# Kernel tuning notes

Hardware: AMD Instinct MI355X
Metric: run time of the kernel (lower is better)

The kernel has to match this reference:

```python
import jax, jax.numpy as jnp
import numpy as np

B, S, D, E, K = 4, 4096, 2048, 64, 8

def setup_inputs() -> dict:
    key = jax.random.key(0)
    k1, k2 = jax.random.split(key, 2)
    x = jax.random.normal(k1, (B, S, D), dtype=jnp.float32)
    # centroid projection params (Dense(features=n_experts))
    W = jax.random.normal(k2, (D, E), dtype=jnp.float32) / np.sqrt(D).astype(np.float32)
    b = jnp.zeros((E,), dtype=jnp.float32)
    return {"x": x, "W": W, "b": b, "k": K}

def reference(x, W, b, k):
    # dense gating projection + sigmoid -> per-token expert scores [B,S,E]
    scores = jax.nn.sigmoid(jnp.einsum('bsd,de->bse', x, W) + b)
    # per-token top-k expert selection (vectorized form of apply_along_axis(top))
    g_i, idx = jax.lax.top_k(scores, k)          # [B,S,k]
    g = g_i / jnp.sum(g_i, axis=-1, keepdims=True)  # renormalize top-k gates
    return g, idx, scores
```

## Files before the change

kernel.cpp:

```cpp
#include <hip/hip_runtime.h>
#include <math.h>
#include <stdint.h>

#define NTOK   16384
#define DDIM   2048
#define NE     64
#define TOPK   8

#define THREADS 512
#define NWAVE   8
#define TOKPB   32
#define BK      64
#define NCHUNK  (DDIM / BK)
#define KSLICE  (BK / NWAVE)

#define XSLOTS   ((BK / 4) * TOKPB)
#define WSLOTS   (BK * (NE / 4))
#define BUFSLOTS (XSLOTS + WSLOTS)

#define SBIDX(t,e) ((t)*67 + ((e) ^ ((t) & 7)))

__device__ __forceinline__ void gl_lds16(const void* g, void* l) {
    __builtin_amdgcn_global_load_lds(
        (const __attribute__((address_space(1))) void*)(uintptr_t)g,
        (__attribute__((address_space(3))) void*)(uintptr_t)l,
        16, 0, 0);
}

__global__ __launch_bounds__(THREADS, 2) void gate_kernel(
    const float* __restrict__ x, const float* __restrict__ W,
    const float* __restrict__ b, float* __restrict__ out)
{
    __shared__ float4 smem[2 * BUFSLOTS];

    const int tid  = threadIdx.x;
    const int wave = tid >> 6;
    const int lane = tid & 63;
    const int tg   = lane >> 3;
    const int eg   = lane & 7;
    const int tok0 = blockIdx.x * TOKPB;

    const int st_k4 = tid >> 5;
    const int st_sg = lane & 31;
    const int st_t  = 4 * (st_sg & 7) + (st_sg >> 3);
    const float* gx  = x + (size_t)(tok0 + st_t) * DDIM + st_k4 * 4;
    const float* gw0 = W + (size_t)(wave * 128 + lane) * 4;
    const float* gw1 = gw0 + 64 * 4;

    float acc[4][8];
#pragma unroll
    for (int i = 0; i < 4; ++i)
#pragma unroll
        for (int j = 0; j < 8; ++j) acc[i][j] = 0.f;

    auto stage = [&](int c) {
        float4* B = &smem[(c & 1) * BUFSLOTS];
        const int kc = c * BK;
        gl_lds16(gx + kc,             &B[wave * 64]);
        gl_lds16(gw0 + (size_t)kc * NE, &B[XSLOTS + wave * 128]);
        gl_lds16(gw1 + (size_t)kc * NE, &B[XSLOTS + wave * 128 + 64]);
    };

    stage(0);
    __syncthreads();

    for (int c = 0; c < NCHUNK; ++c) {
        if (c + 1 < NCHUNK) stage(c + 1);
        const float4* BX = &smem[(c & 1) * BUFSLOTS];
        const float4* BW = BX + XSLOTS;
#pragma unroll
        for (int g = 0; g < 2; ++g) {
            const int k4 = wave * 2 + g;
            float4 xv[4];
#pragma unroll
            for (int i = 0; i < 4; ++i)
                xv[i] = BX[k4 * 32 + tg + 8 * i];
#pragma unroll
            for (int kk = 0; kk < 4; ++kk) {
                const int k = k4 * 4 + kk;
                const float4 wa = BW[k * 16 + eg * 2];
                const float4 wb = BW[k * 16 + eg * 2 + 1];
                const float ws[8] = {wa.x, wa.y, wa.z, wa.w,
                                     wb.x, wb.y, wb.z, wb.w};
#pragma unroll
                for (int i = 0; i < 4; ++i) {
                    const float xs = ((const float*)&xv[i])[kk];
#pragma unroll
                    for (int j = 0; j < 8; ++j)
                        acc[i][j] = fmaf(xs, ws[j], acc[i][j]);
                }
            }
        }
        __syncthreads();
    }

    float* sb = (float*)smem;
    for (int s = tid; s < TOKPB * 67; s += THREADS) sb[s] = 0.f;
    __syncthreads();
#pragma unroll
    for (int i = 0; i < 4; ++i)
#pragma unroll
        for (int j = 0; j < 8; ++j)
            atomicAdd(&sb[SBIDX(tg * 4 + i, eg * 8 + j)], acc[i][j]);
    __syncthreads();

    float* out_g   = out;
    float* out_idx = out + (size_t)NTOK * TOPK;
    float* out_s   = out + (size_t)NTOK * TOPK * 2;

#pragma unroll
    for (int r = 0; r < (TOKPB * NE) / THREADS; ++r) {
        const int flat = r * THREADS + tid;
        const int t = flat >> 6;
        const int e = flat & 63;
        const float z = sb[SBIDX(t, e)] + b[e];
        const float s = 1.f / (1.f + expf(-z));
        out_s[(size_t)tok0 * NE + flat] = s;
        sb[SBIDX(t, e)] = s;
    }
    __syncthreads();

    if (tid < TOKPB) {
        const int t = tid;
        float gv[TOPK];
        int   gi[TOPK];
        float sum = 0.f;
#pragma unroll
        for (int j = 0; j < TOPK; ++j) {
            float best = -1.f;
            int bi = 0;
            for (int e = 0; e < NE; ++e) {
                const float v = sb[SBIDX(t, e)];
                if (v > best) { best = v; bi = e; }
            }
            gv[j] = best; gi[j] = bi; sum += best;
            sb[SBIDX(t, bi)] = -2.f;
        }
        const float inv = 1.f / sum;
#pragma unroll
        for (int j = 0; j < TOPK; ++j) {
            out_g[(size_t)(tok0 + t) * TOPK + j]   = gv[j] * inv;
            out_idx[(size_t)(tok0 + t) * TOPK + j] = (float)gi[j];
        }
    }
}

extern "C" void kernel_launch(void* const* d_in, const int* in_sizes, int n_in,
                              void* d_out, int out_size, void* d_ws, size_t ws_size,
                              hipStream_t stream) {
    const float* x = (const float*)d_in[0];
    const float* W = (const float*)d_in[1];
    const float* b = (const float*)d_in[2];
    float* out = (float*)d_out;
    gate_kernel<<<NTOK / TOKPB, THREADS, 0, stream>>>(x, W, b, out);
}
```

Before: 262.2 us.

## Split k-slices across half-waves with 8x8 per-thread register tile and swizzled W

```diff
diff --git a/kernel.cpp b/kernel.cpp
--- a/kernel.cpp
+++ b/kernel.cpp
@@ -12,10 +12,9 @@
 #define TOKPB   32
 #define BK      64
 #define NCHUNK  (DDIM / BK)
-#define KSLICE  (BK / NWAVE)
 
-#define XSLOTS   ((BK / 4) * TOKPB)
-#define WSLOTS   (BK * (NE / 4))
+#define XSLOTS   512
+#define WSLOTS   1024
 #define BUFSLOTS (XSLOTS + WSLOTS)
 
 #define SBIDX(t,e) ((t)*67 + ((e) ^ ((t) & 7)))
@@ -36,29 +35,33 @@
     const int tid  = threadIdx.x;
     const int wave = tid >> 6;
     const int lane = tid & 63;
-    const int tg   = lane >> 3;
+    const int half = lane >> 5;
+    const int tg   = (lane >> 3) & 3;
     const int eg   = lane & 7;
+    const int k4   = wave * 2 + half;
     const int tok0 = blockIdx.x * TOKPB;
 
-    const int st_k4 = tid >> 5;
-    const int st_sg = lane & 31;
-    const int st_t  = 4 * (st_sg & 7) + (st_sg >> 3);
-    const float* gx  = x + (size_t)(tok0 + st_t) * DDIM + st_k4 * 4;
-    const float* gw0 = W + (size_t)(wave * 128 + lane) * 4;
-    const float* gw1 = gw0 + 64 * 4;
+    const int st_t = (tid & 3) * 8 + ((tid >> 2) & 7);
+    const float* gx = x + (size_t)(tok0 + st_t) * DDIM + ((tid >> 5) << 2);
+    const int s0 = wave * 128 + lane;
+    const int k0 = s0 >> 4, e40 = (s0 & 15) ^ ((k0 >> 2) & 1);
+    const int s1 = s0 + 64;
+    const int k1 = s1 >> 4, e41 = (s1 & 15) ^ ((k1 >> 2) & 1);
+    const float* gw0 = W + (size_t)k0 * NE + e40 * 4;
+    const float* gw1 = W + (size_t)k1 * NE + e41 * 4;
 
-    float acc[4][8];
+    float acc[8][8];
 #pragma unroll
-    for (int i = 0; i < 4; ++i)
+    for (int i = 0; i < 8; ++i)
 #pragma unroll
         for (int j = 0; j < 8; ++j) acc[i][j] = 0.f;
 
     auto stage = [&](int c) {
         float4* B = &smem[(c & 1) * BUFSLOTS];
         const int kc = c * BK;
-        gl_lds16(gx + kc,             &B[wave * 64]);
-        gl_lds16(gw0 + (size_t)kc * NE, &B[XSLOTS + wave * 128]);
-        gl_lds16(gw1 + (size_t)kc * NE, &B[XSLOTS + wave * 128 + 64]);
+        gl_lds16(gx + kc,                    &B[wave * 64]);
+        gl_lds16(gw0 + (size_t)kc * NE,      &B[XSLOTS + wave * 128]);
+        gl_lds16(gw1 + (size_t)kc * NE,      &B[XSLOTS + wave * 128 + 64]);
     };
 
     stage(0);
@@ -68,27 +71,25 @@
         if (c + 1 < NCHUNK) stage(c + 1);
         const float4* BX = &smem[(c & 1) * BUFSLOTS];
         const float4* BW = BX + XSLOTS;
+
+        float4 xv[8];
 #pragma unroll
-        for (int g = 0; g < 2; ++g) {
-            const int k4 = wave * 2 + g;
-            float4 xv[4];
+        for (int i = 0; i < 8; ++i)
+            xv[i] = BX[k4 * 32 + i * 4 + tg];
+
 #pragma unroll
-            for (int i = 0; i < 4; ++i)
-                xv[i] = BX[k4 * 32 + tg + 8 * i];
+        for (int kk = 0; kk < 4; ++kk) {
+            const int k = k4 * 4 + kk;
+            const float4 wa = BW[k * 16 + eg * 2 + half];
+            const float4 wb = BW[k * 16 + eg * 2 + 1 - half];
+            const float ws[8] = {wa.x, wa.y, wa.z, wa.w,
+                                 wb.x, wb.y, wb.z, wb.w};
 #pragma unroll
-            for (int kk = 0; kk < 4; ++kk) {
-                const int k = k4 * 4 + kk;
-                const float4 wa = BW[k * 16 + eg * 2];
-                const float4 wb = BW[k * 16 + eg * 2 + 1];
-                const float ws[8] = {wa.x, wa.y, wa.z, wa.w,
-                                     wb.x, wb.y, wb.z, wb.w};
+            for (int i = 0; i < 8; ++i) {
+                const float xs = ((const float*)&xv[i])[kk];
 #pragma unroll
-                for (int i = 0; i < 4; ++i) {
-                    const float xs = ((const float*)&xv[i])[kk];
-#pragma unroll
-                    for (int j = 0; j < 8; ++j)
-                        acc[i][j] = fmaf(xs, ws[j], acc[i][j]);
-                }
+                for (int j = 0; j < 8; ++j)
+                    acc[i][j] = fmaf(xs, ws[j], acc[i][j]);
             }
         }
         __syncthreads();
@@ -98,10 +99,10 @@
     for (int s = tid; s < TOKPB * 67; s += THREADS) sb[s] = 0.f;
     __syncthreads();
 #pragma unroll
-    for (int i = 0; i < 4; ++i)
+    for (int i = 0; i < 8; ++i)
 #pragma unroll
         for (int j = 0; j < 8; ++j)
-            atomicAdd(&sb[SBIDX(tg * 4 + i, eg * 8 + j)], acc[i][j]);
+            atomicAdd(&sb[SBIDX(tg * 8 + i, eg * 8 + j)], acc[i][j]);
     __syncthreads();
 
     float* out_g   = out;
```

New measurement: 351.3 us. 1.34x slower.
